# Optimization experiments

Hardware: AMD Instinct MI355X
Metric: run time of the kernel (lower is better)

Reference implementation:

```python
import jax, jax.numpy as jnp
import numpy as np

IMAGE_SIZE = 512


def setup_inputs() -> dict:
    key = jax.random.key(0)
    k1, k2, k3, k4, k5 = jax.random.split(key, 5)
    B, S, C, P = 64, IMAGE_SIZE, 64, IMAGE_SIZE * IMAGE_SIZE
    x = jax.random.normal(k1, (B, S, S), dtype=jnp.float32)
    pattern_importance = jax.random.uniform(k2, (B, C), dtype=jnp.float32)
    idxx = jax.random.randint(k3, (P,), 0, S)
    idxy = jax.random.randint(k4, (P,), 0, S)
    cluster_id = jax.random.randint(k5, (P,), 0, C)
    return {"x": x, "pattern_importance": pattern_importance,
            "idxx": idxx, "idxy": idxy, "cluster_id": cluster_id}


def reference(x, pattern_importance, idxx, idxy, cluster_id):
    S = IMAGE_SIZE
    # fft2 with zero-pad/crop to (S, S), then shift DC to center
    x_fft = jnp.fft.fftshift(jnp.fft.fft2(x, s=(S, S), axes=(-2, -1)), axes=(-2, -1))
    # mask: ones everywhere, per-cluster importance scattered at clustered freq bins
    B = x.shape[0]
    mask = jnp.ones((B, S, S), dtype=x.dtype)
    # mask[j, idxx, idxy] = pattern_importance[j, cluster_id] for all batches j at once
    mask = mask.at[:, idxx, idxy].set(pattern_importance[:, cluster_id])
    x_reject = x_fft * mask
    x_ifft = jnp.real(jnp.fft.ifft2(jnp.fft.ifftshift(x_reject, axes=(-2, -1)),
                                    s=(x.shape[1], x.shape[2]), axes=(-2, -1)))
    return x_ifft
```

## Files before the change

kernel.cpp:

```cpp
#include <hip/hip_runtime.h>

#define INV_N2 (1.0f/262144.0f)
#define RS 264
#define TS 520
#define YH_F2 ((size_t)32768 * RS)

typedef unsigned u32x2 __attribute__((ext_vector_type(2)));

__device__ __forceinline__ int brev9(int v) { return (int)(__brev((unsigned)v) >> 23); }
__device__ __forceinline__ float hsin(float rev) { return __builtin_amdgcn_sinf(rev); }
__device__ __forceinline__ float hcos(float rev) { return __builtin_amdgcn_cosf(rev); }

template<int CTRL>
__device__ __forceinline__ float xdpp(float x) {
  int v = __float_as_int(x);
  return __int_as_float(__builtin_amdgcn_update_dpp(v, v, CTRL, 0xF, 0xF, true));
}
__device__ __forceinline__ float xs1(float x) { return xdpp<0xB1>(x); }
__device__ __forceinline__ float xs2(float x) { return xdpp<0x4E>(x); }
__device__ __forceinline__ float xs8(float x) { return xdpp<0x128>(x); }
__device__ __forceinline__ float xs4(float x) {
  return __int_as_float(__builtin_amdgcn_ds_swizzle(__float_as_int(x), 0x101F));
}
__device__ __forceinline__ float xs16(float x) {
#if __has_builtin(__builtin_amdgcn_permlane16_swap)
  u32x2 r = __builtin_amdgcn_permlane16_swap(__float_as_uint(x), __float_as_uint(x), false, false);
  return __uint_as_float((threadIdx.x & 16) ? r[0] : r[1]);
#else
  return __int_as_float(__builtin_amdgcn_ds_swizzle(__float_as_int(x), 0x401F));
#endif
}
__device__ __forceinline__ float xs32(float x) {
#if __has_builtin(__builtin_amdgcn_permlane32_swap)
  u32x2 r = __builtin_amdgcn_permlane32_swap(__float_as_uint(x), __float_as_uint(x), false, false);
  return __uint_as_float((threadIdx.x & 32) ? r[0] : r[1]);
#else
  return __shfl_xor(x, 32, 64);
#endif
}

struct Tw { float c[8], s[8]; };
__device__ __forceinline__ Tw make_tw(int lane) {
  Tw t;
  float a0 = (float)lane        * (1.0f/512.0f);
  float a1 = (float)lane        * (1.0f/256.0f);
  float a2 = (float)lane        * (1.0f/128.0f);
  float a3 = (float)(lane & 31) * (1.0f/64.0f);
  float a4 = (float)(lane & 15) * (1.0f/32.0f);
  float a5 = (float)(lane & 7)  * (1.0f/16.0f);
  float a6 = (float)(lane & 3)  * (1.0f/8.0f);
  float a7 = (float)(lane & 1)  * (1.0f/4.0f);
  t.c[0]=hcos(a0); t.s[0]=hsin(a0); t.c[1]=hcos(a1); t.s[1]=hsin(a1);
  t.c[2]=hcos(a2); t.s[2]=hsin(a2); t.c[3]=hcos(a3); t.s[3]=hsin(a3);
  t.c[4]=hcos(a4); t.s[4]=hsin(a4); t.c[5]=hcos(a5); t.s[5]=hsin(a5);
  t.c[6]=hcos(a6); t.s[6]=hsin(a6); t.c[7]=hcos(a7); t.s[7]=hsin(a7);
  return t;
}

__device__ __forceinline__ void bfly_dif(float &ar, float &ai, float &br, float &bi,
                                         float wr, float wi) {
  float sr = ar + br, si = ai + bi;
  float dr = ar - br, di = ai - bi;
  ar = sr; ai = si;
  br = dr*wr - di*wi; bi = dr*wi + di*wr;
}
__device__ __forceinline__ void bfly_dit(float &ar, float &ai, float &br, float &bi,
                                         float wr, float wi) {
  float tr = br*wr - bi*wi, ti = br*wi + bi*wr;
  br = ar - tr; bi = ai - ti;
  ar = ar + tr; ai = ai + ti;
}

#define FWD_XSTAGE(S, XCHG, CC, SS) { \
  const bool up = (lane & (S)) != 0; \
  const float sg = up ? -1.0f : 1.0f; \
  const float wr = up ? (CC) : 1.0f; \
  const float wi = up ? -(SS) : 0.0f; \
  _Pragma("unroll") for (int k = 0; k < 8; ++k) { \
    float rr = XCHG(xr[k]); float ri = XCHG(xi[k]); \
    float vr = fmaf(sg, xr[k], rr); float vi = fmaf(sg, xi[k], ri); \
    xr[k] = vr*wr - vi*wi; xi[k] = vr*wi + vi*wr; } }

#define INV_XSTAGE(S, XCHG, CC, SS) { \
  const bool up = (lane & (S)) != 0; \
  const float wr = up ? (CC) : 1.0f; \
  const float wi = up ? (SS) : 0.0f; \
  const float sg = up ? -1.0f : 1.0f; \
  _Pragma("unroll") for (int k = 0; k < 8; ++k) { \
    float zr = xr[k]*wr - xi[k]*wi; \
    float zi = xr[k]*wi + xi[k]*wr; \
    float rr = XCHG(zr); float ri = XCHG(zi); \
    xr[k] = fmaf(sg, zr, rr); xi[k] = fmaf(sg, zi, ri); } }

__device__ __forceinline__ void wave_fft512_fwd(float xr[8], float xi[8], int lane,
                                                const Tw& t) {
  {
    float wr = t.c[0], wi = -t.s[0];
    const float rr8 = 0.70710678118654752f, ri8 = -0.70710678118654752f;
    #pragma unroll
    for (int k = 0; k < 4; ++k) {
      bfly_dif(xr[k], xi[k], xr[k+4], xi[k+4], wr, wi);
      float nr = wr*rr8 - wi*ri8, ni = wr*ri8 + wi*rr8;
      wr = nr; wi = ni;
    }
  }
  {
    float w0r = t.c[1], w0i = -t.s[1];
    float w1r = -t.s[1], w1i = -t.c[1];
    bfly_dif(xr[0], xi[0], xr[2], xi[2], w0r, w0i);
    bfly_dif(xr[1], xi[1], xr[3], xi[3], w1r, w1i);
    bfly_dif(xr[4], xi[4], xr[6], xi[6], w0r, w0i);
    bfly_dif(xr[5], xi[5], xr[7], xi[7], w1r, w1i);
  }
  {
    bfly_dif(xr[0], xi[0], xr[1], xi[1], t.c[2], -t.s[2]);
    bfly_dif(xr[2], xi[2], xr[3], xi[3], t.c[2], -t.s[2]);
    bfly_dif(xr[4], xi[4], xr[5], xi[5], t.c[2], -t.s[2]);
    bfly_dif(xr[6], xi[6], xr[7], xi[7], t.c[2], -t.s[2]);
  }
  FWD_XSTAGE(32, xs32, t.c[3], t.s[3])
  FWD_XSTAGE(16, xs16, t.c[4], t.s[4])
  FWD_XSTAGE(8,  xs8,  t.c[5], t.s[5])
  FWD_XSTAGE(4,  xs4,  t.c[6], t.s[6])
  FWD_XSTAGE(2,  xs2,  t.c[7], t.s[7])
  {
    const float sg = (lane & 1) ? -1.0f : 1.0f;
    #pragma unroll
    for (int k = 0; k < 8; ++k) {
      float rr = xs1(xr[k]); float ri = xs1(xi[k]);
      xr[k] = fmaf(sg, xr[k], rr); xi[k] = fmaf(sg, xi[k], ri);
    }
  }
}

__device__ __forceinline__ void wave_fft512_inv(float xr[8], float xi[8], int lane,
                                                const Tw& t) {
  {
    const float sg = (lane & 1) ? -1.0f : 1.0f;
    #pragma unroll
    for (int k = 0; k < 8; ++k) {
      float rr = xs1(xr[k]); float ri = xs1(xi[k]);
      xr[k] = fmaf(sg, xr[k], rr); xi[k] = fmaf(sg, xi[k], ri);
    }
  }
  INV_XSTAGE(2,  xs2,  t.c[7], t.s[7])
  INV_XSTAGE(4,  xs4,  t.c[6], t.s[6])
  INV_XSTAGE(8,  xs8,  t.c[5], t.s[5])
  INV_XSTAGE(16, xs16, t.c[4], t.s[4])
  INV_XSTAGE(32, xs32, t.c[3], t.s[3])
  {
    bfly_dit(xr[0], xi[0], xr[1], xi[1], t.c[2], t.s[2]);
    bfly_dit(xr[2], xi[2], xr[3], xi[3], t.c[2], t.s[2]);
    bfly_dit(xr[4], xi[4], xr[5], xi[5], t.c[2], t.s[2]);
    bfly_dit(xr[6], xi[6], xr[7], xi[7], t.c[2], t.s[2]);
  }
  {
    float w0r = t.c[1], w0i = t.s[1];
    float w1r = -t.s[1], w1i = t.c[1];
    bfly_dit(xr[0], xi[0], xr[2], xi[2], w0r, w0i);
    bfly_dit(xr[1], xi[1], xr[3], xi[3], w1r, w1i);
    bfly_dit(xr[4], xi[4], xr[6], xi[6], w0r, w0i);
    bfly_dit(xr[5], xi[5], xr[7], xi[7], w1r, w1i);
  }
  {
    float wr = t.c[0], wi = t.s[0];
    const float rr8 = 0.70710678118654752f, ri8 = 0.70710678118654752f;
    #pragma unroll
    for (int k = 0; k < 4; ++k) {
      bfly_dit(xr[k], xi[k], xr[k+4], xi[k+4], wr, wi);
      float nr = wr*rr8 - wi*ri8, ni = wr*ri8 + wi*rr8;
      wr = nr; wi = ni;
    }
  }
}

__global__ void k_scatter(const int* __restrict__ idxx, const int* __restrict__ idxy,
                          const int* __restrict__ cid, int* __restrict__ W) {
  int p = blockIdx.x * 256 + threadIdx.x;
  int u = (idxx[p] + 256) & 511;
  int v = (idxy[p] + 256) & 511;
  atomicMax(&W[u * 512 + v], (p << 6) | cid[p]);
}

__global__ void k_pack(const int* __restrict__ W, int* __restrict__ pk) {
  int idx = blockIdx.x * 256 + threadIdx.x;
  if (idx >= 264 * 512) return;
  int j = idx >> 9, n = idx & 511;
  int out = (127 << 7) | 127;
  if (j < 257) {
    int v = (j == 256) ? 256 : brev9(2 * j);
    int u = brev9(n);
    int c1 = W[u * 512 + v];
    int c2 = W[((512 - u) & 511) * 512 + ((512 - v) & 511)];
    int a = (c1 < 0) ? 127 : (c1 & 63);
    int b = (c2 < 0) ? 127 : (c2 & 63);
    out = (b << 7) | a;
  }
  pk[j * 512 + n] = out;
}

__global__ __launch_bounds__(512) void k_fwd_rows(const float* __restrict__ x,
                                                  float2* __restrict__ Yh) {
  __shared__ float zre[8 * 512], zim[8 * 512];
  int tid = threadIdx.x, w = tid >> 6, lane = tid & 63;
  int rp = blockIdx.x * 8 + w;
  const float* rowA = x + (size_t)(2 * rp) * 512;
  const float* rowB = rowA + 512;
  Tw t = make_tw(lane);
  float xr[8], xi[8];
  #pragma unroll
  for (int k = 0; k < 8; ++k) { xr[k] = rowA[k*64 + lane]; xi[k] = rowB[k*64 + lane]; }
  wave_fft512_fwd(xr, xi, lane, t);
  float* zr = zre + w * 512;
  float* zi = zim + w * 512;
  #pragma unroll
  for (int k = 0; k < 8; ++k) { zr[k*64 + lane] = xr[k]; zi[k*64 + lane] = xi[k]; }
  float2* orowA = Yh + (size_t)(2 * rp) * RS;
  float2* orowB = orowA + RS;
  #pragma unroll
  for (int k = 0; k < 4; ++k) {
    int j = k * 64 + lane;
    int n2 = 2 * j;
    int kf = brev9(n2);
    int m = brev9((512 - kf) & 511);
    float er = zr[n2], ei = zi[n2];
    float mr = zr[m],  mi = zi[m];
    orowA[j] = make_float2(0.5f * (er + mr), 0.5f * (ei - mi));
    orowB[j] = make_float2(0.5f * (ei + mi), 0.5f * (mr - er));
  }
  if (lane == 0) {
    orowA[256] = make_float2(zr[1], 0.0f);
    orowB[256] = make_float2(zi[1], 0.0f);
  }
}

__global__ __launch_bounds__(512) void k_cols(float2* __restrict__ Yh,
                                              const int* __restrict__ pk,
                                              const float* __restrict__ pimp) {
  __shared__ float lre[8 * TS], lim[8 * TS];
  __shared__ float pilx[128];
  int tid = threadIdx.x;
  int b = blockIdx.x / 33, g = blockIdx.x % 33;
  float2* base = Yh + (size_t)b * 512 * RS + g * 8;
  #pragma unroll
  for (int rep = 0; rep < 4; ++rep) {
    int m = rep * 512 + tid;
    int i = m >> 2, cp = m & 3;
    float4 v = *(const float4*)(base + (size_t)i * RS + 2 * cp);
    lre[(2*cp)  *TS + i] = v.x; lim[(2*cp)  *TS + i] = v.y;
    lre[(2*cp+1)*TS + i] = v.z; lim[(2*cp+1)*TS + i] = v.w;
  }
  if (tid < 128) pilx[tid] = (tid < 64) ? pimp[b * 64 + tid] : 1.0f;
  int lane = tid & 63;
  Tw t = make_tw(lane);
  __syncthreads();
  int w = tid >> 6;
  float xr[8], xi[8];
  #pragma unroll
  for (int k = 0; k < 8; ++k) {
    xr[k] = lre[w*TS + k*64 + lane];
    xi[k] = lim[w*TS + k*64 + lane];
  }
  wave_fft512_fwd(xr, xi, lane, t);
  const int* cm = pk + (g * 8 + w) * 512;
  #pragma unroll
  for (int k = 0; k < 8; ++k) {
    int p = cm[k*64 + lane];
    float mm = 0.5f * (pilx[p & 127] + pilx[(p >> 7) & 127]) * INV_N2;
    xr[k] *= mm; xi[k] *= mm;
  }
  wave_fft512_inv(xr, xi, lane, t);
  #pragma unroll
  for (int k = 0; k < 8; ++k) {
    lre[w*TS + k*64 + lane] = xr[k];
    lim[w*TS + k*64 + lane] = xi[k];
  }
  __syncthreads();
  #pragma unroll
  for (int rep = 0; rep < 4; ++rep) {
    int m = rep * 512 + tid;
    int i = m >> 2, cp = m & 3;
    *(float4*)(base + (size_t)i * RS + 2 * cp) =
      make_float4(lre[(2*cp)*TS + i], lim[(2*cp)*TS + i],
                  lre[(2*cp+1)*TS + i], lim[(2*cp+1)*TS + i]);
  }
}

__global__ __launch_bounds__(512) void k_inv_rows(const float2* __restrict__ Yh,
                                                  float* __restrict__ out) {
  __shared__ float aRe[8*264], aIm[8*264], bRe[8*264], bIm[8*264];
  int tid = threadIdx.x, w = tid >> 6, lane = tid & 63;
  int rp = blockIdx.x * 8 + w;
  const float2* rowA = Yh + (size_t)(2 * rp) * RS;
  const float2* rowB = rowA + RS;
  Tw t = make_tw(lane);
  float* ar_ = aRe + w*264; float* ai_ = aIm + w*264;
  float* br_ = bRe + w*264; float* bi_ = bIm + w*264;
  #pragma unroll
  for (int k2 = 0; k2 < 5; ++k2) {
    int idx = k2 * 64 + lane;
    if (idx < 257) {
      float2 va = rowA[idx]; ar_[idx] = va.x; ai_[idx] = va.y;
      float2 vb = rowB[idx]; br_[idx] = vb.x; bi_[idx] = vb.y;
    }
  }
  float xr[8], xi[8];
  #pragma unroll
  for (int k = 0; k < 8; ++k) {
    int n = k * 64 + lane;
    int v9 = brev9(n);
    int j2 = brev9((512 - v9) & 511) >> 1;
    bool oddx = (n & 1) && (n != 1);
    int j = (n & 1) ? ((n == 1) ? 256 : j2) : (n >> 1);
    float s = oddx ? -1.0f : 1.0f;
    float ar = ar_[j], ai = ai_[j], br = br_[j], bi = bi_[j];
    xr[k] = ar - s * bi;
    xi[k] = fmaf(s, ai, br);
  }
  wave_fft512_inv(xr, xi, lane, t);
  float* orowA = out + (size_t)(2 * rp) * 512;
  float* orowB = orowA + 512;
  #pragma unroll
  for (int k = 0; k < 8; ++k) {
    orowA[k*64 + lane] = xr[k];
    orowB[k*64 + lane] = xi[k];
  }
}

extern "C" void kernel_launch(void* const* d_in, const int* in_sizes, int n_in,
                              void* d_out, int out_size, void* d_ws, size_t ws_size,
                              hipStream_t stream) {
  const float* x    = (const float*)d_in[0];
  const float* pimp = (const float*)d_in[1];
  const int* idxx   = (const int*)d_in[2];
  const int* idxy   = (const int*)d_in[3];
  const int* cid    = (const int*)d_in[4];

  float2* Yh = (float2*)d_ws;
  int* W  = (int*)((char*)d_ws + YH_F2 * sizeof(float2));
  int* pk = W + 512 * 512;

  hipMemsetAsync(W, 0xFF, 512 * 512 * sizeof(int), stream);
  k_scatter  <<<1024, 256, 0, stream>>>(idxx, idxy, cid, W);
  k_pack     <<<(264 * 512 + 255) / 256, 256, 0, stream>>>(W, pk);
  k_fwd_rows <<<2048, 512, 0, stream>>>(x, Yh);
  k_cols     <<<64 * 33, 512, 0, stream>>>(Yh, pk, pimp);
  k_inv_rows <<<2048, 512, 0, stream>>>(Yh, (float*)d_out);
}
```

Measured before the change: 214.0 us.

## Store row-FFT output transposed so column FFTs read contiguous columns

```diff
diff --git a/kernel.cpp b/kernel.cpp
--- a/kernel.cpp
+++ b/kernel.cpp
@@ -1,9 +1,8 @@
 #include <hip/hip_runtime.h>
 
 #define INV_N2 (1.0f/262144.0f)
-#define RS 264
-#define TS 520
-#define YH_F2 ((size_t)32768 * RS)
+#define TP 17
+#define YT_B ((size_t)(264 * 512))
 
 typedef unsigned u32x2 __attribute__((ext_vector_type(2)));
 
@@ -22,20 +21,24 @@
 __device__ __forceinline__ float xs4(float x) {
   return __int_as_float(__builtin_amdgcn_ds_swizzle(__float_as_int(x), 0x101F));
 }
-__device__ __forceinline__ float xs16(float x) {
+__device__ __forceinline__ void swp16(float x, float &lo, float &hi) {
 #if __has_builtin(__builtin_amdgcn_permlane16_swap)
   u32x2 r = __builtin_amdgcn_permlane16_swap(__float_as_uint(x), __float_as_uint(x), false, false);
-  return __uint_as_float((threadIdx.x & 16) ? r[0] : r[1]);
+  lo = __uint_as_float(r[0]); hi = __uint_as_float(r[1]);
 #else
-  return __int_as_float(__builtin_amdgcn_ds_swizzle(__float_as_int(x), 0x401F));
+  float p = __int_as_float(__builtin_amdgcn_ds_swizzle(__float_as_int(x), 0x401F));
+  bool up = (threadIdx.x & 16) != 0;
+  lo = up ? p : x; hi = up ? x : p;
 #endif
 }
-__device__ __forceinline__ float xs32(float x) {
+__device__ __forceinline__ void swp32(float x, float &lo, float &hi) {
 #if __has_builtin(__builtin_amdgcn_permlane32_swap)
   u32x2 r = __builtin_amdgcn_permlane32_swap(__float_as_uint(x), __float_as_uint(x), false, false);
-  return __uint_as_float((threadIdx.x & 32) ? r[0] : r[1]);
+  lo = __uint_as_float(r[0]); hi = __uint_as_float(r[1]);
 #else
-  return __shfl_xor(x, 32, 64);
+  float p = __shfl_xor(x, 32, 64);
+  bool up = (threadIdx.x & 32) != 0;
+  lo = up ? p : x; hi = up ? x : p;
 #endif
 }
 
@@ -81,6 +84,17 @@
     float vr = fmaf(sg, xr[k], rr); float vi = fmaf(sg, xi[k], ri); \
     xr[k] = vr*wr - vi*wi; xi[k] = vr*wi + vi*wr; } }
 
+#define FWD_SWSTAGE(S, SWP, CC, SS) { \
+  const bool up = (lane & (S)) != 0; \
+  const float sg = up ? -1.0f : 1.0f; \
+  const float wr = up ? (CC) : 1.0f; \
+  const float wi = up ? -(SS) : 0.0f; \
+  _Pragma("unroll") for (int k = 0; k < 8; ++k) { \
+    float lr, hr, li, hi2; \
+    SWP(xr[k], lr, hr); SWP(xi[k], li, hi2); \
+    float vr = fmaf(sg, hr, lr); float vi = fmaf(sg, hi2, li); \
+    xr[k] = vr*wr - vi*wi; xi[k] = vr*wi + vi*wr; } }
+
 #define INV_XSTAGE(S, XCHG, CC, SS) { \
   const bool up = (lane & (S)) != 0; \
   const float wr = up ? (CC) : 1.0f; \
@@ -92,6 +106,18 @@
     float rr = XCHG(zr); float ri = XCHG(zi); \
     xr[k] = fmaf(sg, zr, rr); xi[k] = fmaf(sg, zi, ri); } }
 
+#define INV_SWSTAGE(S, SWP, CC, SS) { \
+  const bool up = (lane & (S)) != 0; \
+  const float wr = up ? (CC) : 1.0f; \
+  const float wi = up ? (SS) : 0.0f; \
+  const float sg = up ? -1.0f : 1.0f; \
+  _Pragma("unroll") for (int k = 0; k < 8; ++k) { \
+    float zr = xr[k]*wr - xi[k]*wi; \
+    float zi = xr[k]*wi + xi[k]*wr; \
+    float lr, hr, li, hi2; \
+    SWP(zr, lr, hr); SWP(zi, li, hi2); \
+    xr[k] = fmaf(sg, hr, lr); xi[k] = fmaf(sg, hi2, li); } }
+
 __device__ __forceinline__ void wave_fft512_fwd(float xr[8], float xi[8], int lane,
                                                 const Tw& t) {
   {
@@ -118,8 +144,8 @@
     bfly_dif(xr[4], xi[4], xr[5], xi[5], t.c[2], -t.s[2]);
     bfly_dif(xr[6], xi[6], xr[7], xi[7], t.c[2], -t.s[2]);
   }
-  FWD_XSTAGE(32, xs32, t.c[3], t.s[3])
-  FWD_XSTAGE(16, xs16, t.c[4], t.s[4])
+  FWD_SWSTAGE(32, swp32, t.c[3], t.s[3])
+  FWD_SWSTAGE(16, swp16, t.c[4], t.s[4])
   FWD_XSTAGE(8,  xs8,  t.c[5], t.s[5])
   FWD_XSTAGE(4,  xs4,  t.c[6], t.s[6])
   FWD_XSTAGE(2,  xs2,  t.c[7], t.s[7])
@@ -146,8 +172,8 @@
   INV_XSTAGE(2,  xs2,  t.c[7], t.s[7])
   INV_XSTAGE(4,  xs4,  t.c[6], t.s[6])
   INV_XSTAGE(8,  xs8,  t.c[5], t.s[5])
-  INV_XSTAGE(16, xs16, t.c[4], t.s[4])
-  INV_XSTAGE(32, xs32, t.c[3], t.s[3])
+  INV_SWSTAGE(16, swp16, t.c[4], t.s[4])
+  INV_SWSTAGE(32, swp32, t.c[3], t.s[3])
   {
     bfly_dit(xr[0], xi[0], xr[1], xi[1], t.c[2], t.s[2]);
     bfly_dit(xr[2], xi[2], xr[3], xi[3], t.c[2], t.s[2]);
@@ -200,23 +226,25 @@
 }
 
 __global__ __launch_bounds__(512) void k_fwd_rows(const float* __restrict__ x,
-                                                  float2* __restrict__ Yh) {
-  __shared__ float zre[8 * 512], zim[8 * 512];
+                                                  float2* __restrict__ Yt) {
+  __shared__ float sm[2 * 264 * TP];
+  float* tR = sm;
+  float* tI = sm + 264 * TP;
   int tid = threadIdx.x, w = tid >> 6, lane = tid & 63;
-  int rp = blockIdx.x * 8 + w;
-  const float* rowA = x + (size_t)(2 * rp) * 512;
+  int R0 = blockIdx.x * 16;
+  int bb = R0 >> 9, r0 = R0 & 511;
+  const float* rowA = x + (size_t)(R0 + 2 * w) * 512;
   const float* rowB = rowA + 512;
   Tw t = make_tw(lane);
   float xr[8], xi[8];
   #pragma unroll
   for (int k = 0; k < 8; ++k) { xr[k] = rowA[k*64 + lane]; xi[k] = rowB[k*64 + lane]; }
   wave_fft512_fwd(xr, xi, lane, t);
-  float* zr = zre + w * 512;
-  float* zi = zim + w * 512;
+  float* zr = sm + w * 1024;
+  float* zi = zr + 512;
   #pragma unroll
   for (int k = 0; k < 8; ++k) { zr[k*64 + lane] = xr[k]; zi[k*64 + lane] = xi[k]; }
-  float2* orowA = Yh + (size_t)(2 * rp) * RS;
-  float2* orowB = orowA + RS;
+  float ar[4], ai[4], br[4], bi[4];
   #pragma unroll
   for (int k = 0; k < 4; ++k) {
     int j = k * 64 + lane;
@@ -225,85 +253,82 @@
     int m = brev9((512 - kf) & 511);
     float er = zr[n2], ei = zi[n2];
     float mr = zr[m],  mi = zi[m];
-    orowA[j] = make_float2(0.5f * (er + mr), 0.5f * (ei - mi));
-    orowB[j] = make_float2(0.5f * (ei + mi), 0.5f * (mr - er));
+    ar[k] = 0.5f * (er + mr); ai[k] = 0.5f * (ei - mi);
+    br[k] = 0.5f * (ei + mi); bi[k] = 0.5f * (mr - er);
+  }
+  float a256 = zr[1], b256 = zi[1];
+  __syncthreads();
+  #pragma unroll
+  for (int k = 0; k < 4; ++k) {
+    int j = k * 64 + lane;
+    tR[j*TP + 2*w]     = ar[k]; tI[j*TP + 2*w]     = ai[k];
+    tR[j*TP + 2*w + 1] = br[k]; tI[j*TP + 2*w + 1] = bi[k];
   }
   if (lane == 0) {
-    orowA[256] = make_float2(zr[1], 0.0f);
-    orowB[256] = make_float2(zi[1], 0.0f);
-  }
-}
-
-__global__ __launch_bounds__(512) void k_cols(float2* __restrict__ Yh,
+    tR[256*TP + 2*w]     = a256; tI[256*TP + 2*w]     = 0.0f;
+    tR[256*TP + 2*w + 1] = b256; tI[256*TP + 2*w + 1] = 0.0f;
+  }
+  __syncthreads();
+  #pragma unroll
+  for (int rep = 0; rep < 9; ++rep) {
+    int e = rep * 512 + tid;
+    int j = e >> 4, rr = e & 15;
+    if (j < 257)
+      Yt[((size_t)bb * 264 + j) * 512 + r0 + rr] =
+        make_float2(tR[j*TP + rr], tI[j*TP + rr]);
+  }
+}
+
+__global__ __launch_bounds__(512) void k_cols(float2* __restrict__ Yt,
                                               const int* __restrict__ pk,
                                               const float* __restrict__ pimp) {
-  __shared__ float lre[8 * TS], lim[8 * TS];
   __shared__ float pilx[128];
   int tid = threadIdx.x;
   int b = blockIdx.x / 33, g = blockIdx.x % 33;
-  float2* base = Yh + (size_t)b * 512 * RS + g * 8;
-  #pragma unroll
-  for (int rep = 0; rep < 4; ++rep) {
-    int m = rep * 512 + tid;
-    int i = m >> 2, cp = m & 3;
-    float4 v = *(const float4*)(base + (size_t)i * RS + 2 * cp);
-    lre[(2*cp)  *TS + i] = v.x; lim[(2*cp)  *TS + i] = v.y;
-    lre[(2*cp+1)*TS + i] = v.z; lim[(2*cp+1)*TS + i] = v.w;
-  }
   if (tid < 128) pilx[tid] = (tid < 64) ? pimp[b * 64 + tid] : 1.0f;
-  int lane = tid & 63;
+  int w = tid >> 6, lane = tid & 63;
+  int j = g * 8 + w;
+  float2* col = Yt + ((size_t)b * 264 + j) * 512;
+  const int* cm = pk + j * 512;
+  int pcm[8];
+  float xr[8], xi[8];
+  #pragma unroll
+  for (int k = 0; k < 8; ++k) {
+    float2 v = col[k*64 + lane];
+    xr[k] = v.x; xi[k] = v.y;
+    pcm[k] = cm[k*64 + lane];
+  }
+  Tw t = make_tw(lane);
+  wave_fft512_fwd(xr, xi, lane, t);
+  __syncthreads();
+  #pragma unroll
+  for (int k = 0; k < 8; ++k) {
+    int p = pcm[k];
+    float mm = 0.5f * (pilx[p & 127] + pilx[(p >> 7) & 127]) * INV_N2;
+    xr[k] *= mm; xi[k] *= mm;
+  }
+  wave_fft512_inv(xr, xi, lane, t);
+  #pragma unroll
+  for (int k = 0; k < 8; ++k) col[k*64 + lane] = make_float2(xr[k], xi[k]);
+}
+
+__global__ __launch_bounds__(512) void k_inv_rows(const float2* __restrict__ Yt,
+                                                  float* __restrict__ out) {
+  __shared__ float tR[264 * TP], tI[264 * TP];
+  int tid = threadIdx.x, w = tid >> 6, lane = tid & 63;
+  int R0 = blockIdx.x * 16;
+  int bb = R0 >> 9, r0 = R0 & 511;
+  #pragma unroll
+  for (int rep = 0; rep < 9; ++rep) {
+    int e = rep * 512 + tid;
+    int j = e >> 4, rr = e & 15;
+    if (j < 257) {
+      float2 v = Yt[((size_t)bb * 264 + j) * 512 + r0 + rr];
+      tR[j*TP + rr] = v.x; tI[j*TP + rr] = v.y;
+    }
+  }
   Tw t = make_tw(lane);
   __syncthreads();
-  int w = tid >> 6;
-  float xr[8], xi[8];
-  #pragma unroll
-  for (int k = 0; k < 8; ++k) {
-    xr[k] = lre[w*TS + k*64 + lane];
-    xi[k] = lim[w*TS + k*64 + lane];
-  }
-  wave_fft512_fwd(xr, xi, lane, t);
-  const int* cm = pk + (g * 8 + w) * 512;
-  #pragma unroll
-  for (int k = 0; k < 8; ++k) {
-    int p = cm[k*64 + lane];
-    float mm = 0.5f * (pilx[p & 127] + pilx[(p >> 7) & 127]) * INV_N2;
-    xr[k] *= mm; xi[k] *= mm;
-  }
-  wave_fft512_inv(xr, xi, lane, t);
-  #pragma unroll
-  for (int k = 0; k < 8; ++k) {
-    lre[w*TS + k*64 + lane] = xr[k];
-    lim[w*TS + k*64 + lane] = xi[k];
-  }
-  __syncthreads();
-  #pragma unroll
-  for (int rep = 0; rep < 4; ++rep) {
-    int m = rep * 512 + tid;
-    int i = m >> 2, cp = m & 3;
-    *(float4*)(base + (size_t)i * RS + 2 * cp) =
-      make_float4(lre[(2*cp)*TS + i], lim[(2*cp)*TS + i],
-                  lre[(2*cp+1)*TS + i], lim[(2*cp+1)*TS + i]);
-  }
-}
-
-__global__ __launch_bounds__(512) void k_inv_rows(const float2* __restrict__ Yh,
-                                                  float* __restrict__ out) {
-  __shared__ float aRe[8*264], aIm[8*264], bRe[8*264], bIm[8*264];
-  int tid = threadIdx.x, w = tid >> 6, lane = tid & 63;
-  int rp = blockIdx.x * 8 + w;
-  const float2* rowA = Yh + (size_t)(2 * rp) * RS;
-  const float2* rowB = rowA + RS;
-  Tw t = make_tw(lane);
-  float* ar_ = aRe + w*264; float* ai_ = aIm + w*264;
-  float* br_ = bRe + w*264; float* bi_ = bIm + w*264;
-  #pragma unroll
-  for (int k2 = 0; k2 < 5; ++k2) {
-    int idx = k2 * 64 + lane;
-    if (idx < 257) {
-      float2 va = rowA[idx]; ar_[idx] = va.x; ai_[idx] = va.y;
-      float2 vb = rowB[idx]; br_[idx] = vb.x; bi_[idx] = vb.y;
-    }
-  }
   float xr[8], xi[8];
   #pragma unroll
   for (int k = 0; k < 8; ++k) {
@@ -313,12 +338,13 @@
     bool oddx = (n & 1) && (n != 1);
     int j = (n & 1) ? ((n == 1) ? 256 : j2) : (n >> 1);
     float s = oddx ? -1.0f : 1.0f;
-    float ar = ar_[j], ai = ai_[j], br = br_[j], bi = bi_[j];
+    float ar = tR[j*TP + 2*w],     ai = tI[j*TP + 2*w];
+    float br = tR[j*TP + 2*w + 1], bi = tI[j*TP + 2*w + 1];
     xr[k] = ar - s * bi;
     xi[k] = fmaf(s, ai, br);
   }
   wave_fft512_inv(xr, xi, lane, t);
-  float* orowA = out + (size_t)(2 * rp) * 512;
+  float* orowA = out + (size_t)(R0 + 2 * w) * 512;
   float* orowB = orowA + 512;
   #pragma unroll
   for (int k = 0; k < 8; ++k) {
@@ -336,14 +362,14 @@
   const int* idxy   = (const int*)d_in[3];
   const int* cid    = (const int*)d_in[4];
 
-  float2* Yh = (float2*)d_ws;
-  int* W  = (int*)((char*)d_ws + YH_F2 * sizeof(float2));
+  float2* Yt = (float2*)d_ws;
+  int* W  = (int*)((char*)d_ws + (size_t)64 * YT_B * sizeof(float2));
   int* pk = W + 512 * 512;
 
   hipMemsetAsync(W, 0xFF, 512 * 512 * sizeof(int), stream);
   k_scatter  <<<1024, 256, 0, stream>>>(idxx, idxy, cid, W);
   k_pack     <<<(264 * 512 + 255) / 256, 256, 0, stream>>>(W, pk);
-  k_fwd_rows <<<2048, 512, 0, stream>>>(x, Yh);
-  k_cols     <<<64 * 33, 512, 0, stream>>>(Yh, pk, pimp);
-  k_inv_rows <<<2048, 512, 0, stream>>>(Yh, (float*)d_out);
-}
+  k_fwd_rows <<<2048, 512, 0, stream>>>(x, Yt);
+  k_cols     <<<64 * 33, 512, 0, stream>>>(Yt, pk, pimp);
+  k_inv_rows <<<2048, 512, 0, stream>>>(Yt, (float*)d_out);
+}
```

Result: faster. 200.7 us (-6.2%).
